# Kernel tuning notes

Hardware: AMD Instinct MI355X
Metric: run time of the kernel (lower is better)

Reference implementation:

```python
import jax, jax.numpy as jnp
import numpy as np

N, E, IN, HID, OUT, H, NCLS = 20000, 320000, 128, 32, 8, 8, 10

def _ln(x, g, b, eps=1e-5):
    mu = x.mean(-1, keepdims=True)
    var = ((x - mu) ** 2).mean(-1, keepdims=True)
    return g * (x - mu) / jnp.sqrt(var + eps) + b

def _gelu(x):
    return jax.nn.gelu(x, approximate=False)

def _tconv(x, src, dst, Wq, bq, Wk, bk, Wv, bv, Ws, bs, heads):
    # PyG TransformerConv, concat=True, root_weight=True, lin_beta is None
    n = x.shape[0]
    C = Wq.shape[1] // heads
    q = (x @ Wq + bq).reshape(n, heads, C)
    k = (x @ Wk + bk).reshape(n, heads, C)
    v = (x @ Wv + bv).reshape(n, heads, C)
    logits = (q[dst] * k[src]).sum(-1) / jnp.sqrt(jnp.asarray(C, x.dtype))  # [E,H]
    m = jax.lax.stop_gradient(jax.ops.segment_max(logits, dst, num_segments=n))
    e = jnp.exp(logits - m[dst])
    denom = jax.ops.segment_sum(e, dst, num_segments=n)
    alpha = e / (denom[dst] + 1e-16)  # per-target-node edge softmax
    agg = jax.ops.segment_sum(alpha[:, :, None] * v[src], dst, num_segments=n)
    out = agg.reshape(n, heads * C) + x @ Ws + bs
    return out, alpha

def _forward(src, dst, x,
             c1_Wq, c1_bq, c1_Wk, c1_bk, c1_Wv, c1_bv, c1_Ws, c1_bs,
             c2_Wq, c2_bq, c2_Wk, c2_bk, c2_Wv, c2_bv, c2_Ws, c2_bs,
             c3_Wq, c3_bq, c3_Wk, c3_bk, c3_Wv, c3_bv, c3_Ws, c3_bs,
             c4_Wq, c4_bq, c4_Wk, c4_bk, c4_Wv, c4_bv, c4_Ws, c4_bs,
             n1_g, n1_b, n2_g, n2_b, n3_g, n3_b, n4_g, n4_b,
             fc_W, fc_b):
    h1 = _ln(_gelu(_tconv(x, src, dst, c1_Wq, c1_bq, c1_Wk, c1_bk, c1_Wv, c1_bv, c1_Ws, c1_bs, H)[0]), n1_g, n1_b)
    h2_raw, attn = _tconv(h1, src, dst, c2_Wq, c2_bq, c2_Wk, c2_bk, c2_Wv, c2_bv, c2_Ws, c2_bs, H)
    h2 = _ln(_gelu(h2_raw), n2_g, n2_b)
    h3 = _ln(_gelu(_tconv(h2, src, dst, c3_Wq, c3_bq, c3_Wk, c3_bk, c3_Wv, c3_bv, c3_Ws, c3_bs, H)[0]), n3_g, n3_b)
    h4 = _ln(_gelu(_tconv(h3, src, dst, c4_Wq, c4_bq, c4_Wk, c4_bk, c4_Wv, c4_bv, c4_Ws, c4_bs, 1)[0]), n4_g, n4_b)
    x_out = h2 @ fc_W + fc_b
    return x_out, h4, attn

def setup_inputs() -> dict:
    key = jax.random.key(0)
    ks = iter(jax.random.split(key, 64))
    def p(shape, s=0.05):
        return jax.random.normal(next(ks), shape, dtype=jnp.float32) * s
    inp = {}
    inp['x'] = jax.random.normal(next(ks), (N, IN), dtype=jnp.float32)
    inp['edge_index'] = jax.random.randint(next(ks), (2, E), 0, N, dtype=jnp.int32)
    dims = [('c1', IN, H * HID), ('c2', H * HID, H * OUT), ('c3', H * OUT, H * HID), ('c4', H * HID, IN)]
    for name, di, do in dims:
        for w in ['Wq', 'Wk', 'Wv', 'Ws']:
            inp[name + '_' + w] = p((di, do))
        for bnm in ['bq', 'bk', 'bv', 'bs']:
            inp[name + '_' + bnm] = jnp.zeros((do,), jnp.float32)
    for nm, d in [('n1', H * HID), ('n2', H * OUT), ('n3', H * HID), ('n4', IN)]:
        inp[nm + '_g'] = jnp.ones((d,), jnp.float32)
        inp[nm + '_b'] = jnp.zeros((d,), jnp.float32)
    inp['fc_W'] = p((H * OUT, NCLS))
    inp['fc_b'] = jnp.zeros((NCLS,), jnp.float32)
    return inp

def reference(x, edge_index,
              c1_Wq, c1_bq, c1_Wk, c1_bk, c1_Wv, c1_bv, c1_Ws, c1_bs,
              c2_Wq, c2_bq, c2_Wk, c2_bk, c2_Wv, c2_bv, c2_Ws, c2_bs,
              c3_Wq, c3_bq, c3_Wk, c3_bk, c3_Wv, c3_bv, c3_Ws, c3_bs,
              c4_Wq, c4_bq, c4_Wk, c4_bk, c4_Wv, c4_bv, c4_Ws, c4_bs,
              n1_g, n1_b, n2_g, n2_b, n3_g, n3_b, n4_g, n4_b,
              fc_W, fc_b):
    src, dst = edge_index[0], edge_index[1]
    return _forward(src, dst, x,
                    c1_Wq, c1_bq, c1_Wk, c1_bk, c1_Wv, c1_bv, c1_Ws, c1_bs,
                    c2_Wq, c2_bq, c2_Wk, c2_bk, c2_Wv, c2_bv, c2_Ws, c2_bs,
                    c3_Wq, c3_bq, c3_Wk, c3_bk, c3_Wv, c3_bv, c3_Ws, c3_bs,
                    c4_Wq, c4_bq, c4_Wk, c4_bk, c4_Wv, c4_bv, c4_Ws, c4_bs,
                    n1_g, n1_b, n2_g, n2_b, n3_g, n3_b, n4_g, n4_b,
                    fc_W, fc_b)
```

## Files before the change

kernel.cpp:

```cpp
#include <hip/hip_runtime.h>
#include <hip/hip_bf16.h>
#include <math.h>

#define NN 20000
#define MP 20032
#define NE 320000

typedef __hip_bfloat16 bf16;
typedef __attribute__((ext_vector_type(8))) short short8v;
typedef __attribute__((ext_vector_type(4))) short short4v;
typedef __attribute__((ext_vector_type(4))) float f32x4;

__device__ __forceinline__ float b2f(bf16 v){ return __bfloat162float(v); }
__device__ __forceinline__ bf16 f2b(float v){ return __float2bfloat16(v); }
__device__ __forceinline__ float bfbits(short s){
  return __uint_as_float(((unsigned)(unsigned short)s) << 16);
}
__device__ __forceinline__ int clampi(int v, int lo, int hi){ return v < lo ? lo : (v > hi ? hi : v); }
__device__ __forceinline__ void stv(bf16* p, float v){ *p = f2b(v); }
__device__ __forceinline__ void stv(float* p, float v){ *p = v; }
__device__ __forceinline__ float ldv(const bf16* p){ return b2f(*p); }
__device__ __forceinline__ float ldv(const float* p){ return *p; }

template<int CPL>
__device__ __forceinline__ void ldrow(const bf16* p, float* o){
  if constexpr (CPL == 16){
    short8v v0 = *reinterpret_cast<const short8v*>(p);
    short8v v1 = *reinterpret_cast<const short8v*>(p + 8);
#pragma unroll
    for (int j = 0; j < 8; j++){ o[j] = bfbits(v0[j]); o[8+j] = bfbits(v1[j]); }
  } else if constexpr (CPL == 8){
    short8v v = *reinterpret_cast<const short8v*>(p);
#pragma unroll
    for (int j = 0; j < 8; j++) o[j] = bfbits(v[j]);
  } else {
    short4v v = *reinterpret_cast<const short4v*>(p);
#pragma unroll
    for (int j = 0; j < 4; j++) o[j] = bfbits(v[j]);
  }
}

__device__ __forceinline__ short8v ldA8(const bf16* p){
  return *reinterpret_cast<const short8v*>(p);
}
__device__ __forceinline__ short8v ldA8(const float* p){
  float4 a0 = *reinterpret_cast<const float4*>(p);
  float4 a1 = *reinterpret_cast<const float4*>(p + 4);
  short8v r;
  bf16 b;
  b = f2b(a0.x); r[0] = *(const short*)&b;
  b = f2b(a0.y); r[1] = *(const short*)&b;
  b = f2b(a0.z); r[2] = *(const short*)&b;
  b = f2b(a0.w); r[3] = *(const short*)&b;
  b = f2b(a1.x); r[4] = *(const short*)&b;
  b = f2b(a1.y); r[5] = *(const short*)&b;
  b = f2b(a1.z); r[6] = *(const short*)&b;
  b = f2b(a1.w); r[7] = *(const short*)&b;
  return r;
}

__global__ void fill_k(float* __restrict__ out, int n, float val){
  int i = blockIdx.x*blockDim.x + threadIdx.x;
  if (i < n) out[i] = val;
}

struct PackArgs {
  const float* w[16];
  unsigned long long off[16];
  int K[16];
  int D[16];
};
__global__ void pack_all(PackArgs pa, bf16* __restrict__ out){
  int wi = blockIdx.y;
  int K = pa.K[wi], D = pa.D[wi];
  int i = blockIdx.x*256 + threadIdx.x;
  if (i >= K*D) return;
  int j = i & 7, l = (i >> 3) & 63;
  int TG = D >> 4;
  int tg = (i >> 9) % TG, s = (i >> 9) / TG;
  int k = s*32 + (l >> 4)*8 + j, n = tg*16 + (l & 15);
  out[pa.off[wi] + i] = f2b(pa.w[wi][(size_t)k*D + n]);
}

template<typename AT, typename TS>
__global__ void gemm_qkvs(const AT* __restrict__ X,
    const short8v* __restrict__ WQ, const short8v* __restrict__ WK,
    const short8v* __restrict__ WV, const short8v* __restrict__ WS,
    const float* __restrict__ bQ, const float* __restrict__ bK,
    const float* __restrict__ bV, const float* __restrict__ bS,
    bf16* __restrict__ Qo, bf16* __restrict__ Ko, bf16* __restrict__ Vo,
    TS* __restrict__ So,
    int K, int TG, int ldQKV, int ldS, int MstoreS){
  int w = threadIdx.x >> 6, lane = threadIdx.x & 63;
  int n0 = blockIdx.x*64;
  size_t m0 = (size_t)blockIdx.y*64 + w*16;
  int lr = lane & 15, lk = lane >> 4;
  int ar = clampi((int)(m0 + lr), 0, NN-1);
  const AT* xp = X + (size_t)ar*K + lk*8;
  size_t wo = ((size_t)(n0 >> 4))*64 + lane;
  f32x4 acc[4][4];
#pragma unroll
  for (int j = 0; j < 4; j++)
#pragma unroll
    for (int t = 0; t < 4; t++) acc[j][t] = f32x4{0,0,0,0};
  int steps = K >> 5;
  for (int s = 0; s < steps; s++){
    short8v a = ldA8(xp + s*32);
    size_t ro = wo + (size_t)s*TG*64;
#pragma unroll
    for (int t = 0; t < 4; t++){
      size_t idx = ro + t*64;
      acc[0][t] = __builtin_amdgcn_mfma_f32_16x16x32_bf16(a, WQ[idx], acc[0][t], 0, 0, 0);
      acc[1][t] = __builtin_amdgcn_mfma_f32_16x16x32_bf16(a, WK[idx], acc[1][t], 0, 0, 0);
      acc[2][t] = __builtin_amdgcn_mfma_f32_16x16x32_bf16(a, WV[idx], acc[2][t], 0, 0, 0);
      acc[3][t] = __builtin_amdgcn_mfma_f32_16x16x32_bf16(a, WS[idx], acc[3][t], 0, 0, 0);
    }
  }
#pragma unroll
  for (int t = 0; t < 4; t++){
    int col = n0 + t*16 + lr;
    float b0 = bQ[col], b1 = bK[col], b2 = bV[col], b3 = bS[col];
#pragma unroll
    for (int r = 0; r < 4; r++){
      size_t row = m0 + lk*4 + r;
      Qo[row*ldQKV + col] = f2b(acc[0][t][r] + b0);
      Ko[row*ldQKV + col] = f2b(acc[1][t][r] + b1);
      Vo[row*ldQKV + col] = f2b(acc[2][t][r] + b2);
      if ((int)row < MstoreS) stv(&So[row*(size_t)ldS + col], acc[3][t][r] + b3);
    }
  }
}

__global__ void count_k(const int* __restrict__ ei, int* __restrict__ cnt, int E){
  int e = blockIdx.x*blockDim.x + threadIdx.x;
  if (e < E){
    int d = clampi(ei[E + e], 0, NN-1);
    atomicAdd(&cnt[d], 1);
  }
}

__global__ void exscan_k(const int* __restrict__ cnt, int* __restrict__ off,
                         int* __restrict__ cur, int n){
  __shared__ int wtot[16];
  __shared__ int carrysh;
  int tid = threadIdx.x, lane = tid & 63, w = tid >> 6;
  if (tid == 0) carrysh = 0;
  __syncthreads();
  for (int base = 0; base < n; base += 1024){
    int i = base + tid;
    int v = (i < n) ? cnt[i] : 0;
    int s = v;
#pragma unroll
    for (int d = 1; d < 64; d <<= 1){
      int t = __shfl_up(s, d);
      if (lane >= d) s += t;
    }
    if (lane == 63) wtot[w] = s;
    __syncthreads();
    int woff = 0;
    for (int j = 0; j < w; j++) woff += wtot[j];
    int c = carrysh;
    if (i < n){ int val = c + woff + s - v; off[i] = val; cur[i] = val; }
    __syncthreads();
    if (tid == 1023) carrysh = c + woff + s;
    __syncthreads();
  }
  if (threadIdx.x == 0) off[n] = carrysh;
}

__global__ void scatter_k(const int* __restrict__ ei, int* __restrict__ cur,
                          int* __restrict__ perm, int* __restrict__ srcs, int E){
  int e = blockIdx.x*blockDim.x + threadIdx.x;
  if (e >= E) return;
  int s = clampi(ei[e], 0, NN-1);
  int d = clampi(ei[E + e], 0, NN-1);
  int p = atomicAdd(&cur[d], 1);
  if (p >= 0 && p < E){ perm[p] = e; srcs[p] = s; }
}

template<int D, int H, typename TO>
__global__ void fused_attn(const bf16* __restrict__ Q, const bf16* __restrict__ Kf,
                           const bf16* __restrict__ V, const int* __restrict__ srcs,
                           const int* __restrict__ offs,
                           TO* __restrict__ Xout, int ldO,
                           bf16* __restrict__ LOG, float* __restrict__ MxO,
                           float* __restrict__ DnO, float scale){
  constexpr int CPL = D/16;
  constexpr int LPH = 16/H;
  int node = blockIdx.x*4 + (threadIdx.x >> 6);
  if (node >= NN) return;
  int lane = threadIdx.x & 63;
  int hl = lane & 15;
  int slot = lane >> 4;
  float q[CPL];
  {
    float tmp[CPL];
    ldrow<CPL>(Q + (size_t)node*D + hl*CPL, tmp);
#pragma unroll
    for (int j = 0; j < CPL; j++) q[j] = tmp[j] * scale;
  }
  float m = -INFINITY, den = 0.f;
  float acc[CPL];
#pragma unroll
  for (int j = 0; j < CPL; j++) acc[j] = 0.f;
  int s0 = offs[node], e0 = offs[node+1];
  int i = s0 + slot;
  bool vcur = i < e0;
  int sc = vcur ? srcs[i] : 0;
  float kc[CPL], vc[CPL];
  ldrow<CPL>(Kf + (size_t)sc*D + hl*CPL, kc);
  ldrow<CPL>(V  + (size_t)sc*D + hl*CPL, vc);
  int iters = (e0 - s0 + 3) >> 2;
  for (int it = 0; it < iters; ++it){
    int inext = i + 4;
    bool vnxt = inext < e0;
    int sn = vnxt ? srcs[inext] : 0;
    float kn[CPL], vn[CPL];
    ldrow<CPL>(Kf + (size_t)sn*D + hl*CPL, kn);
    ldrow<CPL>(V  + (size_t)sn*D + hl*CPL, vn);
    float t = 0.f;
#pragma unroll
    for (int j = 0; j < CPL; j++) t += q[j]*kc[j];
#pragma unroll
    for (int o = 1; o < LPH; o <<= 1) t += __shfl_xor(t, o);
    if (!vcur) t = -INFINITY;
    if (LOG && vcur && ((hl & (LPH-1)) == 0)) LOG[(size_t)i*H + hl/LPH] = f2b(t);
    float tm = fmaxf(t, __shfl_xor(t, 16));
    tm = fmaxf(tm, __shfl_xor(tm, 32));
    float nm = fmaxf(m, tm);
    float fe = __expf(m - nm);
    float pe = __expf(t - nm);
    den = den*fe + pe;
#pragma unroll
    for (int j = 0; j < CPL; j++) acc[j] = acc[j]*fe + pe*vc[j];
    m = nm;
    vcur = vnxt; i = inext;
#pragma unroll
    for (int j = 0; j < CPL; j++){ kc[j] = kn[j]; vc[j] = vn[j]; }
  }
  den += __shfl_xor(den, 16);
  den += __shfl_xor(den, 32);
#pragma unroll
  for (int j = 0; j < CPL; j++){
    acc[j] += __shfl_xor(acc[j], 16);
    acc[j] += __shfl_xor(acc[j], 32);
  }
  float inv = 1.f/(den + 1e-16f);
  if (slot == 0){
    TO* o = Xout + (size_t)node*ldO + hl*CPL;
#pragma unroll
    for (int j = 0; j < CPL; j++) stv(&o[j], ldv(&o[j]) + acc[j]*inv);
    if (MxO && ((hl & (LPH-1)) == 0)){
      MxO[node*H + hl/LPH] = m;
      DnO[node*H + hl/LPH] = den;
    }
  }
}

__global__ void alpha8_k(const bf16* __restrict__ LOG, const float* __restrict__ Mx,
                         const float* __restrict__ Dn, const int* __restrict__ ei,
                         const int* __restrict__ perm, float* __restrict__ attn){
  size_t t = (size_t)blockIdx.x*blockDim.x + threadIdx.x;
  if (t >= (size_t)NE*8) return;
  int pos = (int)(t >> 3), h = (int)(t & 7);
  int e = perm[pos];
  int node = ei[NE + e];
  float a = __expf(b2f(LOG[t]) - Mx[node*8 + h]) / (Dn[node*8 + h] + 1e-16f);
  attn[(size_t)e*8 + h] = a;
}

template<int CPL, typename T>
__global__ void gelu_ln(T* __restrict__ X, const float* __restrict__ G,
                        const float* __restrict__ Bt){
  int node = blockIdx.x*4 + (threadIdx.x >> 6);
  if (node >= NN) return;
  constexpr int D = CPL*64;
  int lane = threadIdx.x & 63;
  T* xr = X + (size_t)node*D + lane*CPL;
  float v[CPL]; float s = 0.f;
#pragma unroll
  for (int j = 0; j < CPL; j++){
    float t = ldv(&xr[j]);
    float ge = 0.5f*t*(1.f + erff(t*0.70710678118654752f));
    v[j] = ge; s += ge;
  }
#pragma unroll
  for (int off = 1; off < 64; off <<= 1) s += __shfl_xor(s, off);
  float mu = s * (1.f/D);
  float q = 0.f;
#pragma unroll
  for (int j = 0; j < CPL; j++){ float d = v[j]-mu; q += d*d; }
#pragma unroll
  for (int off = 1; off < 64; off <<= 1) q += __shfl_xor(q, off);
  float inv = 1.f / sqrtf(q*(1.f/D) + 1e-5f);
#pragma unroll
  for (int j = 0; j < CPL; j++){
    int c = lane*CPL + j;
    stv(&xr[j], G[c]*(v[j]-mu)*inv + Bt[c]);
  }
}

__global__ void fc_k(const bf16* __restrict__ X, const float* __restrict__ W,
                     const float* __restrict__ B, float* __restrict__ Out,
                     int K, int D){
  int m = blockIdx.x*4 + (threadIdx.x >> 6);
  int lane = threadIdx.x & 63;
  if (m >= NN || lane >= D) return;
  float acc = B[lane];
  for (int k = 0; k < K; k++) acc += b2f(X[(size_t)m*K + k]) * W[(size_t)k*D + lane];
  Out[(size_t)m*D + lane] = acc;
}

extern "C" void kernel_launch(void* const* d_in, const int* in_sizes, int n_in,
                              void* d_out, int out_size, void* d_ws, size_t ws_size,
                              hipStream_t stream){
  int code = 0;
  if (n_in != 44) code = 100;
  else {
    const int wsz[4] = {32768,16384,16384,32768};
    const int bsz[4] = {256,64,256,128};
    bool ok = in_sizes[0] == NN*128 && in_sizes[1] == 2*NE
           && in_sizes[42] == 640 && in_sizes[43] == 10;
    for (int l = 0; l < 4 && ok; l++){
      for (int j = 0; j < 4; j++)
        ok = ok && in_sizes[2+l*8+j] == wsz[l] && in_sizes[2+l*8+4+j] == bsz[l];
      ok = ok && in_sizes[34+2*l] == bsz[l] && in_sizes[35+2*l] == bsz[l];
    }
    if (!ok) code = 140;
  }
  if (code){
    fill_k<<<((size_t)out_size+255)/256, 256, 0, stream>>>((float*)d_out, out_size, (float)code);
    return;
  }

  const float* x = (const float*)d_in[0];
  const int*   ei = (const int*)d_in[1];
  const float *W[4][4], *Bw[4][4], *lng[4], *lnb[4];
  for (int l = 0; l < 4; l++){
    for (int j = 0; j < 4; j++){
      W[l][j]  = (const float*)d_in[2 + l*8 + j];
      Bw[l][j] = (const float*)d_in[2 + l*8 + 4 + j];
    }
    lng[l] = (const float*)d_in[34 + 2*l];
    lnb[l] = (const float*)d_in[35 + 2*l];
  }
  const float* fcW = (const float*)d_in[42];
  const float* fcB = (const float*)d_in[43];

  char* ws = (char*)d_ws;
  size_t o = 0;
  auto alloc = [&](size_t bytes)->void*{ void* p = ws + o; o += (bytes + 255)/256*256; return p; };
  bf16* Hb   = (bf16*)alloc((size_t)MP*256*2);
  bf16* H2b  = (bf16*)alloc((size_t)MP*64*2);
  bf16* Qb   = (bf16*)alloc((size_t)MP*256*2);
  bf16* Kb   = (bf16*)alloc((size_t)MP*256*2);
  bf16* Vb   = (bf16*)alloc((size_t)MP*256*2);
  bf16* LOG  = (bf16*)alloc((size_t)NE*8*2);
  float* Mx  = (float*)alloc((size_t)NN*8*4);
  float* Dn  = (float*)alloc((size_t)NN*8*4);
  int* OFFS  = (int*)alloc((size_t)(NN+1)*4);
  int* CNT   = (int*)alloc((size_t)(NN+1)*4);
  int* CURS  = (int*)alloc((size_t)(NN+1)*4);
  int* PERM  = (int*)alloc((size_t)NE*4);
  int* SRCS  = (int*)alloc((size_t)NE*4);
  bf16* WPK  = (bf16*)alloc((size_t)393216*2);
  size_t need = o;

  float* out_x  = (float*)d_out;
  float* out_h4 = out_x + (size_t)NN*10;
  float* out_at = out_h4 + (size_t)NN*128;

  if (ws_size < need){
    fill_k<<<((size_t)out_size+255)/256, 256, 0, stream>>>((float*)d_out, out_size, 160.0f);
    return;
  }

  const int KD[4] = {128,256,64,256};
  const int DD[4] = {256,64,256,128};
  PackArgs pa;
  bf16* Wp[4][4];
  {
    size_t off = 0;
    for (int l = 0; l < 4; l++)
      for (int j = 0; j < 4; j++){
        int idx = l*4 + j;
        pa.w[idx] = W[l][j];
        pa.off[idx] = off;
        pa.K[idx] = KD[l];
        pa.D[idx] = DD[l];
        Wp[l][j] = WPK + off;
        off += (size_t)KD[l]*DD[l];
      }
  }
  pack_all<<<dim3(128,16),256,0,stream>>>(pa, WPK);

  hipMemsetAsync(CNT, 0, (size_t)NN*4, stream);
  count_k<<<NE/256, 256, 0, stream>>>(ei, CNT, NE);
  exscan_k<<<1, 1024, 0, stream>>>(CNT, OFFS, CURS, NN);
  scatter_k<<<NE/256, 256, 0, stream>>>(ei, CURS, PERM, SRCS, NE);

  const float s32  = 0.1767766952966369f;
  const float s8   = 0.3535533905932738f;
  const float s128 = 0.0883883476483184f;
  const dim3 g64(1, MP/64), g128(2, MP/64), g256(4, MP/64);

  gemm_qkvs<float,bf16><<<g256,256,0,stream>>>(x,
      (const short8v*)Wp[0][0], (const short8v*)Wp[0][1],
      (const short8v*)Wp[0][2], (const short8v*)Wp[0][3],
      Bw[0][0], Bw[0][1], Bw[0][2], Bw[0][3],
      Qb, Kb, Vb, Hb, 128, 16, 256, 256, MP);
  fused_attn<256,8,bf16><<<NN/4,256,0,stream>>>(Qb,Kb,Vb, SRCS,OFFS, Hb,256,
                                                nullptr,nullptr,nullptr, s32);
  gelu_ln<4><<<NN/4,256,0,stream>>>(Hb, lng[0], lnb[0]);

  gemm_qkvs<bf16,bf16><<<g64,256,0,stream>>>(Hb,
      (const short8v*)Wp[1][0], (const short8v*)Wp[1][1],
      (const short8v*)Wp[1][2], (const short8v*)Wp[1][3],
      Bw[1][0], Bw[1][1], Bw[1][2], Bw[1][3],
      Qb, Kb, Vb, H2b, 256, 4, 64, 64, MP);
  fused_attn<64,8,bf16><<<NN/4,256,0,stream>>>(Qb,Kb,Vb, SRCS,OFFS, H2b,64,
                                               LOG,Mx,Dn, s8);
  alpha8_k<<<NE*8/256,256,0,stream>>>(LOG, Mx, Dn, ei, PERM, out_at);
  gelu_ln<1><<<NN/4,256,0,stream>>>(H2b, lng[1], lnb[1]);

  fc_k<<<NN/4,256,0,stream>>>(H2b, fcW, fcB, out_x, 64, 10);

  gemm_qkvs<bf16,bf16><<<g256,256,0,stream>>>(H2b,
      (const short8v*)Wp[2][0], (const short8v*)Wp[2][1],
      (const short8v*)Wp[2][2], (const short8v*)Wp[2][3],
      Bw[2][0], Bw[2][1], Bw[2][2], Bw[2][3],
      Qb, Kb, Vb, Hb, 64, 16, 256, 256, MP);
  fused_attn<256,8,bf16><<<NN/4,256,0,stream>>>(Qb,Kb,Vb, SRCS,OFFS, Hb,256,
                                                nullptr,nullptr,nullptr, s32);
  gelu_ln<4><<<NN/4,256,0,stream>>>(Hb, lng[2], lnb[2]);

  gemm_qkvs<bf16,float><<<g128,256,0,stream>>>(Hb,
      (const short8v*)Wp[3][0], (const short8v*)Wp[3][1],
      (const short8v*)Wp[3][2], (const short8v*)Wp[3][3],
      Bw[3][0], Bw[3][1], Bw[3][2], Bw[3][3],
      Qb, Kb, Vb, out_h4, 256, 8, 128, 128, NN);
  fused_attn<128,1,float><<<NN/4,256,0,stream>>>(Qb,Kb,Vb, SRCS,OFFS, out_h4,128,
                                                 nullptr,nullptr,nullptr, s128);
  gelu_ln<2><<<NN/4,256,0,stream>>>(out_h4, lng[3], lnb[3]);
}
```

Measured before the change: 364.4 us.

## Fuse GELU+LayerNorm and alpha output into attention; process nodes in degree order

Folds the GELU+LayerNorm epilogue and the per-edge attention-probability write into the fused attention kernel. This removes three separate elementwise passes per layer and the Mx/Dn intermediates. It also adds a degree-histogram counting sort (hist, scan, order kernels) so that nodes are processed in descending degree order, to balance work across wavefronts. In exchange it adds three small preprocessing launches, and the outputs are written in scattered node order, which makes stores less coalesced.

```diff
diff --git a/kernel.cpp b/kernel.cpp
--- a/kernel.cpp
+++ b/kernel.cpp
@@ -178,17 +178,54 @@
   if (p >= 0 && p < E){ perm[p] = e; srcs[p] = s; }
 }
 
+__global__ void hist_k(const int* __restrict__ cnt, int* __restrict__ hist){
+  int i = blockIdx.x*blockDim.x + threadIdx.x;
+  if (i < NN){
+    int d = cnt[i]; if (d > 511) d = 511;
+    atomicAdd(&hist[d], 1);
+  }
+}
+__global__ void hscan_k(const int* __restrict__ hist, int* __restrict__ hcur){
+  __shared__ int wtot[8];
+  int tid = threadIdx.x;
+  int lane = tid & 63, w = tid >> 6;
+  int d = 511 - tid;
+  int v = hist[d];
+  int s = v;
+#pragma unroll
+  for (int o = 1; o < 64; o <<= 1){
+    int t = __shfl_up(s, o);
+    if (lane >= o) s += t;
+  }
+  if (lane == 63) wtot[w] = s;
+  __syncthreads();
+  int woff = 0;
+  for (int j = 0; j < w; j++) woff += wtot[j];
+  hcur[d] = woff + s - v;
+}
+__global__ void order_k(const int* __restrict__ cnt, int* __restrict__ hcur,
+                        int* __restrict__ order){
+  int i = blockIdx.x*blockDim.x + threadIdx.x;
+  if (i < NN){
+    int d = cnt[i]; if (d > 511) d = 511;
+    int p = atomicAdd(&hcur[d], 1);
+    order[p] = i;
+  }
+}
+
 template<int D, int H, typename TO>
 __global__ void fused_attn(const bf16* __restrict__ Q, const bf16* __restrict__ Kf,
                            const bf16* __restrict__ V, const int* __restrict__ srcs,
-                           const int* __restrict__ offs,
+                           const int* __restrict__ offs, const int* __restrict__ order,
                            TO* __restrict__ Xout, int ldO,
-                           bf16* __restrict__ LOG, float* __restrict__ MxO,
-                           float* __restrict__ DnO, float scale){
+                           const float* __restrict__ G, const float* __restrict__ Bt,
+                           bf16* __restrict__ LOG, const int* __restrict__ perm,
+                           float* __restrict__ attn_out, float scale){
   constexpr int CPL = D/16;
   constexpr int LPH = 16/H;
-  int node = blockIdx.x*4 + (threadIdx.x >> 6);
-  if (node >= NN) return;
+  int gid = blockIdx.x*4 + (threadIdx.x >> 6);
+  if (gid >= NN) return;
+  int node = order[gid];
   int lane = threadIdx.x & 63;
   int hl = lane & 15;
   int slot = lane >> 4;
@@ -246,57 +283,50 @@
     acc[j] += __shfl_xor(acc[j], 32);
   }
   float inv = 1.f/(den + 1e-16f);
-  if (slot == 0){
-    TO* o = Xout + (size_t)node*ldO + hl*CPL;
-#pragma unroll
-    for (int j = 0; j < CPL; j++) stv(&o[j], ldv(&o[j]) + acc[j]*inv);
-    if (MxO && ((hl & (LPH-1)) == 0)){
-      MxO[node*H + hl/LPH] = m;
-      DnO[node*H + hl/LPH] = den;
-    }
-  }
-}
-
-__global__ void alpha8_k(const bf16* __restrict__ LOG, const float* __restrict__ Mx,
-                         const float* __restrict__ Dn, const int* __restrict__ ei,
-                         const int* __restrict__ perm, float* __restrict__ attn){
-  size_t t = (size_t)blockIdx.x*blockDim.x + threadIdx.x;
-  if (t >= (size_t)NE*8) return;
-  int pos = (int)(t >> 3), h = (int)(t & 7);
-  int e = perm[pos];
-  int node = ei[NE + e];
-  float a = __expf(b2f(LOG[t]) - Mx[node*8 + h]) / (Dn[node*8 + h] + 1e-16f);
-  attn[(size_t)e*8 + h] = a;
-}
-
-template<int CPL, typename T>
-__global__ void gelu_ln(T* __restrict__ X, const float* __restrict__ G,
-                        const float* __restrict__ Bt){
-  int node = blockIdx.x*4 + (threadIdx.x >> 6);
-  if (node >= NN) return;
-  constexpr int D = CPL*64;
-  int lane = threadIdx.x & 63;
-  T* xr = X + (size_t)node*D + lane*CPL;
-  float v[CPL]; float s = 0.f;
-#pragma unroll
-  for (int j = 0; j < CPL; j++){
-    float t = ldv(&xr[j]);
-    float ge = 0.5f*t*(1.f + erff(t*0.70710678118654752f));
-    v[j] = ge; s += ge;
-  }
-#pragma unroll
-  for (int off = 1; off < 64; off <<= 1) s += __shfl_xor(s, off);
-  float mu = s * (1.f/D);
-  float q = 0.f;
-#pragma unroll
-  for (int j = 0; j < CPL; j++){ float d = v[j]-mu; q += d*d; }
-#pragma unroll
-  for (int off = 1; off < 64; off <<= 1) q += __shfl_xor(q, off);
-  float inv = 1.f / sqrtf(q*(1.f/D) + 1e-5f);
-#pragma unroll
-  for (int j = 0; j < CPL; j++){
-    int c = lane*CPL + j;
-    stv(&xr[j], G[c]*(v[j]-mu)*inv + Bt[c]);
+
+  {
+    const TO* oin = Xout + (size_t)node*ldO + hl*CPL;
+    float v[CPL]; float s = 0.f;
+#pragma unroll
+    for (int j = 0; j < CPL; j++){
+      float t = ldv(&oin[j]) + acc[j]*inv;
+      float ge = 0.5f*t*(1.f + erff(t*0.70710678118654752f));
+      v[j] = ge; s += ge;
+    }
+#pragma unroll
+    for (int o = 1; o < 16; o <<= 1) s += __shfl_xor(s, o);
+    float mu = s * (1.f/D);
+    float qv = 0.f;
+#pragma unroll
+    for (int j = 0; j < CPL; j++){ float d2 = v[j]-mu; qv += d2*d2; }
+#pragma unroll
+    for (int o = 1; o < 16; o <<= 1) qv += __shfl_xor(qv, o);
+    float lni = 1.f / sqrtf(qv*(1.f/D) + 1e-5f);
+    if (slot == 0){
+      TO* oo = Xout + (size_t)node*ldO + hl*CPL;
+#pragma unroll
+      for (int j = 0; j < CPL; j++){
+        int c = hl*CPL + j;
+        stv(&oo[j], G[c]*(v[j]-mu)*lni + Bt[c]);
+      }
+    }
+  }
+
+  if (attn_out){
+    asm volatile("s_waitcnt vmcnt(0)" ::: "memory");
+    int total = (e0 - s0) * H;
+    int it2 = (total + 63) >> 6;
+    for (int b = 0; b < it2; b++){
+      int idx = b*64 + lane;
+      int h = idx & (H-1);
+      float mh = __shfl(m, h*LPH);
+      float dh = __shfl(den, h*LPH);
+      if (idx < total){
+        int pos = s0 + (idx >> 3);
+        float lg = b2f(LOG[(size_t)pos*H + h]);
+        attn_out[(size_t)perm[pos]*H + h] = __expf(lg - mh)/(dh + 1e-16f);
+      }
+    }
   }
 }
 
@@ -356,13 +386,14 @@
   bf16* Kb   = (bf16*)alloc((size_t)MP*256*2);
   bf16* Vb   = (bf16*)alloc((size_t)MP*256*2);
   bf16* LOG  = (bf16*)alloc((size_t)NE*8*2);
-  float* Mx  = (float*)alloc((size_t)NN*8*4);
-  float* Dn  = (float*)alloc((size_t)NN*8*4);
   int* OFFS  = (int*)alloc((size_t)(NN+1)*4);
   int* CNT   = (int*)alloc((size_t)(NN+1)*4);
   int* CURS  = (int*)alloc((size_t)(NN+1)*4);
   int* PERM  = (int*)alloc((size_t)NE*4);
   int* SRCS  = (int*)alloc((size_t)NE*4);
+  int* HIST  = (int*)alloc(512*4);
+  int* HCUR  = (int*)alloc(512*4);
+  int* ORDER = (int*)alloc((size_t)NN*4);
   bf16* WPK  = (bf16*)alloc((size_t)393216*2);
   size_t need = o;
 
@@ -395,9 +426,13 @@
   pack_all<<<dim3(128,16),256,0,stream>>>(pa, WPK);
 
   hipMemsetAsync(CNT, 0, (size_t)NN*4, stream);
+  hipMemsetAsync(HIST, 0, 512*4, stream);
   count_k<<<NE/256, 256, 0, stream>>>(ei, CNT, NE);
   exscan_k<<<1, 1024, 0, stream>>>(CNT, OFFS, CURS, NN);
   scatter_k<<<NE/256, 256, 0, stream>>>(ei, CURS, PERM, SRCS, NE);
+  hist_k<<<(NN+255)/256, 256, 0, stream>>>(CNT, HIST);
+  hscan_k<<<1, 512, 0, stream>>>(HIST, HCUR);
+  order_k<<<(NN+255)/256, 256, 0, stream>>>(CNT, HCUR, ORDER);
 
   const float s32  = 0.1767766952966369f;
   const float s8   = 0.3535533905932738f;
@@ -409,19 +444,16 @@
       (const short8v*)Wp[0][2], (const short8v*)Wp[0][3],
       Bw[0][0], Bw[0][1], Bw[0][2], Bw[0][3],
       Qb, Kb, Vb, Hb, 128, 16, 256, 256, MP);
-  fused_attn<256,8,bf16><<<NN/4,256,0,stream>>>(Qb,Kb,Vb, SRCS,OFFS, Hb,256,
-                                                nullptr,nullptr,nullptr, s32);
-  gelu_ln<4><<<NN/4,256,0,stream>>>(Hb, lng[0], lnb[0]);
+  fused_attn<256,8,bf16><<<NN/4,256,0,stream>>>(Qb,Kb,Vb, SRCS,OFFS,ORDER, Hb,256,
+      lng[0],lnb[0], nullptr,nullptr,nullptr, s32);
 
   gemm_qkvs<bf16,bf16><<<g64,256,0,stream>>>(Hb,
       (const short8v*)Wp[1][0], (const short8v*)Wp[1][1],
       (const short8v*)Wp[1][2], (const short8v*)Wp[1][3],
       Bw[1][0], Bw[1][1], Bw[1][2], Bw[1][3],
       Qb, Kb, Vb, H2b, 256, 4, 64, 64, MP);
-  fused_attn<64,8,bf16><<<NN/4,256,0,stream>>>(Qb,Kb,Vb, SRCS,OFFS, H2b,64,
-                                               LOG,Mx,Dn, s8);
-  alpha8_k<<<NE*8/256,256,0,stream>>>(LOG, Mx, Dn, ei, PERM, out_at);
-  gelu_ln<1><<<NN/4,256,0,stream>>>(H2b, lng[1], lnb[1]);
+  fused_attn<64,8,bf16><<<NN/4,256,0,stream>>>(Qb,Kb,Vb, SRCS,OFFS,ORDER, H2b,64,
+      lng[1],lnb[1], LOG,PERM,out_at, s8);
 
   fc_k<<<NN/4,256,0,stream>>>(H2b, fcW, fcB, out_x, 64, 10);
 
@@ -430,16 +462,14 @@
       (const short8v*)Wp[2][2], (const short8v*)Wp[2][3],
       Bw[2][0], Bw[2][1], Bw[2][2], Bw[2][3],
       Qb, Kb, Vb, Hb, 64, 16, 256, 256, MP);
-  fused_attn<256,8,bf16><<<NN/4,256,0,stream>>>(Qb,Kb,Vb, SRCS,OFFS, Hb,256,
-                                                nullptr,nullptr,nullptr, s32);
-  gelu_ln<4><<<NN/4,256,0,stream>>>(Hb, lng[2], lnb[2]);
+  fused_attn<256,8,bf16><<<NN/4,256,0,stream>>>(Qb,Kb,Vb, SRCS,OFFS,ORDER, Hb,256,
+      lng[2],lnb[2], nullptr,nullptr,nullptr, s32);
 
   gemm_qkvs<bf16,float><<<g128,256,0,stream>>>(Hb,
       (const short8v*)Wp[3][0], (const short8v*)Wp[3][1],
       (const short8v*)Wp[3][2], (const short8v*)Wp[3][3],
       Bw[3][0], Bw[3][1], Bw[3][2], Bw[3][3],
       Qb, Kb, Vb, out_h4, 256, 8, 128, 128, NN);
-  fused_attn<128,1,float><<<NN/4,256,0,stream>>>(Qb,Kb,Vb, SRCS,OFFS, out_h4,128,
-                                                 nullptr,nullptr,nullptr, s128);
-  gelu_ln<2><<<NN/4,256,0,stream>>>(out_h4, lng[3], lnb[3]);
-}
+  fused_attn<128,1,float><<<NN/4,256,0,stream>>>(Qb,Kb,Vb, SRCS,OFFS,ORDER, out_h4,128,
+      lng[3],lnb[3], nullptr,nullptr,nullptr, s128);
+}
```

Result: slower. 532.3 us (+46.1%).
